# Optimization experiments

Measured on AMD Instinct MI355X. Metric: run time of the kernel, lower is better.

Reference implementation:

```python
import jax, jax.numpy as jnp
import numpy as np

B, L, D, H = 4, 2048, 1024, 16
DH = D // H

def setup_inputs() -> dict:
    key = jax.random.key(0)
    k1, k2, k3 = jax.random.split(key, 3)
    x = jax.random.normal(k1, (B, L, D), dtype=jnp.float32)
    w_qkv = jax.random.normal(k2, (3 * D, D), dtype=jnp.float32) * (1.0 / np.sqrt(D))
    w_proj = jax.random.normal(k3, (D, D), dtype=jnp.float32) * (1.0 / np.sqrt(D))
    return {"x": x, "w_qkv": w_qkv, "w_proj": w_proj}

def reference(x, w_qkv, w_proj):
    b, l, d = x.shape
    scale = 1.0 / np.sqrt(DH)
    qkv = (x @ w_qkv.T).reshape(b, l, 3, H, DH)
    qkv = jnp.transpose(qkv, (2, 0, 3, 1, 4))
    q, k, v = qkv[0], qkv[1], qkv[2]
    scores = jnp.einsum('bhqd,bhkd->bhqk', q, k) * scale
    attn = jax.nn.softmax(scores, axis=-1)
    out = jnp.einsum('bhqk,bhkd->bhqd', attn, v)
    out = jnp.transpose(out, (0, 2, 1, 3)).reshape(b, l, d)
    return out @ w_proj.T
```

## Files before the change

kernel.cpp:

```cpp
#include <hip/hip_runtime.h>
#include <hip/hip_bf16.h>


typedef __bf16  bf16x8  __attribute__((ext_vector_type(8)));
typedef __bf16  bf16x4  __attribute__((ext_vector_type(4)));
typedef float   floatx4 __attribute__((ext_vector_type(4)));

__device__ __forceinline__ void async_ld16(const void* g, void* lds_base_uniform) {
  __builtin_amdgcn_global_load_lds(
      (const __attribute__((address_space(1))) void*)g,
      (__attribute__((address_space(3))) void*)lds_base_uniform,
      16, 0, 0);
}

__device__ __forceinline__ int detect_bf16(const void* p) {
  const unsigned short* u = (const unsigned short*)p;
  int sane = 0;
#pragma unroll 4
  for (int i = 0; i < 64; ++i) {
    unsigned short w = u[2 * i];
    int e = (w >> 7) & 0xFF;
    sane += (w == 0 || (e >= 100 && e <= 150)) ? 1 : 0;
  }
  return sane >= 32;
}

__device__ __forceinline__ bf16x8 ld8_f32cvt(const void* base, size_t elem) {
  const float* p = (const float*)base + elem;
  floatx4 u0 = *(const floatx4*)p;
  floatx4 u1 = *(const floatx4*)(p + 4);
  bf16x8 v;
  v[0] = (__bf16)u0[0]; v[1] = (__bf16)u0[1]; v[2] = (__bf16)u0[2]; v[3] = (__bf16)u0[3];
  v[4] = (__bf16)u1[0]; v[5] = (__bf16)u1[1]; v[6] = (__bf16)u1[2]; v[7] = (__bf16)u1[3];
  return v;
}

template<int CTRL>
__device__ __forceinline__ float dpp_f(float x) {
  return __builtin_bit_cast(float,
      __builtin_amdgcn_update_dpp(0, __builtin_bit_cast(int, x), CTRL, 0xF, 0xF, true));
}
__device__ __forceinline__ float row16_sum(float x) {
  x += dpp_f<0xB1>(x);
  x += dpp_f<0x4E>(x);
  x += dpp_f<0x141>(x);
  x += dpp_f<0x140>(x);
  return x;
}

__launch_bounds__(256)
__global__ void cvt3_kernel(const void* __restrict__ s0, __bf16* __restrict__ d0, int n0,
                            const void* __restrict__ s1, __bf16* __restrict__ d1, int n1,
                            const void* __restrict__ s2, __bf16* __restrict__ d2) {
  int u = blockIdx.x * blockDim.x + threadIdx.x;
  const void* src; __bf16* dst;
  if (u < n0)           { src = s0; dst = d0; }
  else if (u < n0 + n1) { src = s1; dst = d1; u -= n0; }
  else                  { src = s2; dst = d2; u -= n0 + n1; }
  const int is_bf16 = detect_bf16(src);
  const size_t e = (size_t)u * 8;
  if (is_bf16) *(bf16x8*)(dst + e) = *(const bf16x8*)((const __bf16*)src + e);
  else         *(bf16x8*)(dst + e) = ld8_f32cvt(src, e);
}

template<int EPI>
__launch_bounds__(256, 3)
__global__ void gemm_bt_kernel(const __bf16* __restrict__ A,
                               const __bf16* __restrict__ B,
                               const void* __restrict__ oprobe,
                               void* __restrict__ Cout,
                               __bf16* __restrict__ qb,
                               __bf16* __restrict__ kb,
                               __bf16* __restrict__ vtb,
                               int M, int N, int K)
{
  __shared__ __align__(16) __bf16 As[128 * 32];
  __shared__ __align__(16) __bf16 Bs[128 * 32];

  const int flat = blockIdx.x;
  const int m0 = (((flat & 7) << 3) | ((flat >> 3) & 7)) << 7;
  const int n0 = (flat >> 6) << 7;

  const int tid  = threadIdx.x;
  const int wave = tid >> 6;
  const int lane = tid & 63;
  const int quad = lane >> 4;
  const int l16  = lane & 15;
  const int wm   = wave >> 1;
  const int wn   = wave & 1;

  const int r_in   = lane >> 2;
  const int cchunk = lane & 3;

  const __bf16* Ab = A + (size_t)m0 * K;
  const __bf16* Bb = B + (size_t)n0 * K;

  floatx4 acc[4][4];
#pragma unroll
  for (int i = 0; i < 4; ++i)
#pragma unroll
    for (int j = 0; j < 4; ++j)
      acc[i][j] = (floatx4){0.f, 0.f, 0.f, 0.f};

  const int ca0 = wave * 2;
  for (int k0 = 0; k0 < K; k0 += 32) {
#pragma unroll
    for (int i = 0; i < 2; ++i) {
      const int ca  = ca0 + i;
      const int row = ca * 16 + r_in;
      async_ld16(Ab + (size_t)row * K + k0 + cchunk * 8, (char*)As + ca * 1024);
      async_ld16(Bb + (size_t)row * K + k0 + cchunk * 8, (char*)Bs + ca * 1024);
    }
    __syncthreads();

    bf16x8 af[4], bfr[4];
#pragma unroll
    for (int tt = 0; tt < 4; ++tt) {
      af[tt]  = *(const bf16x8*)&As[(wm * 64 + tt * 16 + l16) * 32 + quad * 8];
      bfr[tt] = *(const bf16x8*)&Bs[(wn * 64 + tt * 16 + l16) * 32 + quad * 8];
    }
#pragma unroll
    for (int mt = 0; mt < 4; ++mt)
#pragma unroll
      for (int nt = 0; nt < 4; ++nt)
        acc[mt][nt] = __builtin_amdgcn_mfma_f32_16x16x32_bf16(af[mt], bfr[nt], acc[mt][nt], 0, 0, 0);
    __syncthreads();
  }

  const int out_bf16 = (EPI == 1) ? detect_bf16(oprobe) : 0;

#pragma unroll
  for (int mt = 0; mt < 4; ++mt) {
#pragma unroll
    for (int nt = 0; nt < 4; ++nt) {
      const int n_idx = n0 + wn * 64 + nt * 16 + l16;
      const int mbase = m0 + wm * 64 + mt * 16 + quad * 4;
      if (EPI == 1) {
        if (out_bf16) {
#pragma unroll
          for (int r = 0; r < 4; ++r)
            ((__bf16*)Cout)[(size_t)(mbase + r) * N + n_idx] = (__bf16)acc[mt][nt][r];
        } else {
#pragma unroll
          for (int r = 0; r < 4; ++r)
            ((float*)Cout)[(size_t)(mbase + r) * N + n_idx] = acc[mt][nt][r];
        }
      } else {
        const int sel = n_idx >> 10;
        const int rem = n_idx & 1023;
        const int h   = rem >> 6;
        const int dh  = rem & 63;
        const int b   = mbase >> 11;
        const int l   = mbase & 2047;
        const int bh  = b * 16 + h;
        if (sel == 2) {
          bf16x4 pk;
#pragma unroll
          for (int r = 0; r < 4; ++r) pk[r] = (__bf16)acc[mt][nt][r];
          *(bf16x4*)&vtb[((size_t)bh * 64 + dh) * 2048 + l] = pk;
        } else {
          __bf16* dstb = (sel == 0 ? qb : kb) + ((size_t)bh * 2048 + l) * 64 + dh;
#pragma unroll
          for (int r = 0; r < 4; ++r)
            dstb[(size_t)r * 64] = (__bf16)acc[mt][nt][r];
        }
      }
    }
  }
}

__launch_bounds__(256, 4)
__global__ void attn_kernel(const __bf16* __restrict__ qb,
                            const __bf16* __restrict__ kb,
                            const __bf16* __restrict__ vtb,
                            __bf16* __restrict__ ob )
{
  __shared__ __align__(16) __bf16 S[2][2 * 64 * 72];

  const int tid  = threadIdx.x;
  const int wave = tid >> 6;
  const int lane = tid & 63;
  const int quad = lane >> 4;
  const int l16  = lane & 15;

  const int bh = blockIdx.y;
  const int b  = bh >> 4;
  const int h  = bh & 15;
  const int q0 = blockIdx.x * 128;

  const __bf16* Qp = qb  + (size_t)bh * 2048 * 64;
  const __bf16* Kp = kb  + (size_t)bh * 2048 * 64;
  const __bf16* Vp = vtb + (size_t)bh * 64 * 2048;

  const float C1 = 0.125f * 1.44269504f;
  const float C2 = -8.0f  * 1.44269504f;

  bf16x8 aq[2][2];
#pragma unroll
  for (int rt = 0; rt < 2; ++rt) {
    const __bf16* qrow = Qp + (size_t)(q0 + wave * 32 + rt * 16 + l16) * 64;
    aq[rt][0] = *(const bf16x8*)(qrow + quad * 8);
    aq[rt][1] = *(const bf16x8*)(qrow + 32 + quad * 8);
  }

  bf16x8 onesb;
  {
    const __bf16 ov = (l16 == 0) ? (__bf16)1.0f : (__bf16)0.0f;
#pragma unroll
    for (int i = 0; i < 8; ++i) onesb[i] = ov;
  }

  floatx4 o[2][4], o5[2];
#pragma unroll
  for (int rt = 0; rt < 2; ++rt) {
    o5[rt] = (floatx4){0.f, 0.f, 0.f, 0.f};
#pragma unroll
    for (int dt = 0; dt < 4; ++dt) o[rt][dt] = (floatx4){0.f, 0.f, 0.f, 0.f};
  }

  const int sarr = wave >> 1;
  const int srb  = (wave & 1) * 32;
  const int sr0  = lane >> 3;
  const int scol = (lane & 7) * 8;

  {
    __bf16* dst = &S[0][sarr * (64 * 72)];
    if (sarr == 0) {
#pragma unroll
      for (int i = 0; i < 4; ++i) {
        const int row = srb + sr0 + 8 * i;
        *(bf16x8*)&dst[row * 72 + scol] = *(const bf16x8*)(Kp + (size_t)row * 64 + scol);
      }
    } else {
#pragma unroll
      for (int i = 0; i < 4; ++i) {
        const int row = srb + sr0 + 8 * i;
        *(bf16x8*)&dst[row * 72 + scol] = *(const bf16x8*)(Vp + (size_t)row * 2048 + scol);
      }
    }
  }
  __syncthreads();

  for (int kt = 0; kt < 32; ++kt) {
    const int cur = kt & 1;
    const int nxt = cur ^ 1;
    const int kn  = (((kt + 1) & 31) << 6);

    bf16x8 sreg[4];
    if (sarr == 0) {
#pragma unroll
      for (int i = 0; i < 4; ++i) {
        const int row = srb + sr0 + 8 * i;
        sreg[i] = *(const bf16x8*)(Kp + (size_t)(kn + row) * 64 + scol);
      }
    } else {
#pragma unroll
      for (int i = 0; i < 4; ++i) {
        const int row = srb + sr0 + 8 * i;
        sreg[i] = *(const bf16x8*)(Vp + (size_t)row * 2048 + kn + scol);
      }
    }

    const __bf16* Kc = &S[cur][0];
    const __bf16* Vc = &S[cur][64 * 72];
    __bf16*       Pq = &S[nxt][0] + wave * 2304;

    floatx4 st[2][4];
    __builtin_amdgcn_s_setprio(1);
#pragma unroll
    for (int nt = 0; nt < 4; ++nt) {
      const int krow = nt * 16 + l16;
      bf16x8 ak0 = *(const bf16x8*)&Kc[krow * 72 + quad * 8];
      bf16x8 ak1 = *(const bf16x8*)&Kc[krow * 72 + 32 + quad * 8];
#pragma unroll
      for (int rt = 0; rt < 2; ++rt) {
        floatx4 z = (floatx4){0.f, 0.f, 0.f, 0.f};
        z = __builtin_amdgcn_mfma_f32_16x16x32_bf16(ak0, aq[rt][0], z, 0, 0, 0);
        z = __builtin_amdgcn_mfma_f32_16x16x32_bf16(ak1, aq[rt][1], z, 0, 0, 0);
        st[rt][nt] = z;
      }
    }
    __builtin_amdgcn_s_setprio(0);

#pragma unroll
    for (int rt = 0; rt < 2; ++rt) {
#pragma unroll
      for (int nt = 0; nt < 4; ++nt) {
        bf16x4 pk;
#pragma unroll
        for (int r = 0; r < 4; ++r)
          pk[r] = (__bf16)__builtin_amdgcn_exp2f(fmaf(st[rt][nt][r], C1, C2));
        *(bf16x4*)&Pq[(rt * 16 + l16) * 72 + nt * 16 + quad * 4] = pk;
      }
    }

    __builtin_amdgcn_wave_barrier();

    bf16x8 ap[2][2];
#pragma unroll
    for (int rt = 0; rt < 2; ++rt) {
      ap[rt][0] = *(const bf16x8*)&Pq[(rt * 16 + l16) * 72 + quad * 8];
      ap[rt][1] = *(const bf16x8*)&Pq[(rt * 16 + l16) * 72 + 32 + quad * 8];
    }

    __builtin_amdgcn_s_setprio(1);
#pragma unroll
    for (int dt = 0; dt < 4; ++dt) {
      const int vrow = dt * 16 + l16;
      bf16x8 bv0 = *(const bf16x8*)&Vc[vrow * 72 + quad * 8];
      bf16x8 bv1 = *(const bf16x8*)&Vc[vrow * 72 + 32 + quad * 8];
#pragma unroll
      for (int rt = 0; rt < 2; ++rt) {
        o[rt][dt] = __builtin_amdgcn_mfma_f32_16x16x32_bf16(ap[rt][0], bv0, o[rt][dt], 0, 0, 0);
        o[rt][dt] = __builtin_amdgcn_mfma_f32_16x16x32_bf16(ap[rt][1], bv1, o[rt][dt], 0, 0, 0);
      }
    }
#pragma unroll
    for (int rt = 0; rt < 2; ++rt) {
      o5[rt] = __builtin_amdgcn_mfma_f32_16x16x32_bf16(ap[rt][0], onesb, o5[rt], 0, 0, 0);
      o5[rt] = __builtin_amdgcn_mfma_f32_16x16x32_bf16(ap[rt][1], onesb, o5[rt], 0, 0, 0);
    }
    __builtin_amdgcn_s_setprio(0);

    __builtin_amdgcn_wave_barrier();

    {
      __bf16* dst = &S[nxt][sarr * (64 * 72)];
#pragma unroll
      for (int i = 0; i < 4; ++i) {
        const int row = srb + sr0 + 8 * i;
        *(bf16x8*)&dst[row * 72 + scol] = sreg[i];
      }
    }
    __syncthreads();
  }

#pragma unroll
  for (int rt = 0; rt < 2; ++rt)
#pragma unroll
    for (int r = 0; r < 4; ++r) {
      const float lv  = row16_sum(l16 == 0 ? o5[rt][r] : 0.f);
      const float inv = 1.f / lv;
      const size_t rowbase =
          ((size_t)b * 2048 + q0 + wave * 32 + rt * 16 + quad * 4 + r) * 1024 + h * 64;
#pragma unroll
      for (int dt = 0; dt < 4; ++dt)
        ob[rowbase + dt * 16 + l16] = (__bf16)(o[rt][dt][r] * inv);
    }
}

extern "C" void kernel_launch(void* const* d_in, const int* in_sizes, int n_in,
                              void* d_out, int out_size, void* d_ws, size_t ws_size,
                              hipStream_t stream)
{
  (void)in_sizes; (void)n_in; (void)out_size; (void)ws_size;

  const void* x     = d_in[0];
  const void* wqkv  = d_in[1];
  const void* wproj = d_in[2];

  const size_t NX    = (size_t)8192 * 1024;
  const size_t NWQKV = (size_t)3072 * 1024;
  const size_t NWPRJ = (size_t)1024 * 1024;

  __bf16* qbuf   = (__bf16*)d_ws;
  __bf16* kbuf   = qbuf + NX;
  __bf16* vtbuf  = kbuf + NX;
  __bf16* abuf   = vtbuf + NX;
  __bf16* xb     = abuf + NX;
  __bf16* wqkvb  = xb + NX;
  __bf16* wprojb = wqkvb + NWQKV;

  dim3 blk(256);

  cvt3_kernel<<<dim3((NX + NWQKV + NWPRJ) / 2048), blk, 0, stream>>>(
      x, xb, NX / 8, wqkv, wqkvb, NWQKV / 8, wproj, wprojb);

  gemm_bt_kernel<0><<<dim3(24 * 64), blk, 0, stream>>>(
      xb, wqkvb, nullptr, nullptr, qbuf, kbuf, vtbuf, 8192, 3072, 1024);

  attn_kernel<<<dim3(2048 / 128, 64), blk, 0, stream>>>(qbuf, kbuf, vtbuf, abuf);

  gemm_bt_kernel<1><<<dim3(8 * 64), blk, 0, stream>>>(
      abuf, wprojb, wproj, d_out, nullptr, nullptr, nullptr, 8192, 1024, 1024);
}
```

Measured before the change: 288.1 us.

## Add dedicated 256x256 QKV GEMM kernel with 4-stage async LDS pipeline

```diff
diff --git a/kernel.cpp b/kernel.cpp
--- a/kernel.cpp
+++ b/kernel.cpp
@@ -63,15 +63,115 @@
   else         *(bf16x8*)(dst + e) = ld8_f32cvt(src, e);
 }
 
+__launch_bounds__(512, 2)
+__global__ void gemm_qkv_kernel(const __bf16* __restrict__ A,
+                                const __bf16* __restrict__ B,
+                                __bf16* __restrict__ qb,
+                                __bf16* __restrict__ kb,
+                                __bf16* __restrict__ vtb)
+{
+  __shared__ __align__(16) __bf16 SM[4 * 16384];
+
+  const int flat = blockIdx.x;
+  const int xcd  = flat & 7;
+  const int j    = flat >> 3;
+  const int m0   = ((xcd << 2) | (j & 3)) << 8;
+  const int n0   = (j >> 2) << 8;
+
+  const int tid  = threadIdx.x;
+  const int wave = tid >> 6;
+  const int lane = tid & 63;
+  const int quad = lane >> 4;
+  const int l16  = lane & 15;
+  const int wm   = wave >> 2;
+  const int wn   = wave & 3;
+
+  const int srow = tid >> 2;
+  const int scc  = (((tid & 3) ^ ((tid >> 3) & 3)) << 3);
+
+  auto STAGE = [&](int buf, int k0) {
+    char* base = (char*)SM + buf * 32768;
+#pragma unroll
+    for (int i = 0; i < 2; ++i) {
+      async_ld16(A + (size_t)(m0 + i * 128 + srow) * 1024 + k0 + scc,
+                 base + i * 8192 + wave * 1024);
+      async_ld16(B + (size_t)(n0 + i * 128 + srow) * 1024 + k0 + scc,
+                 base + 16384 + i * 8192 + wave * 1024);
+    }
+  };
+
+  floatx4 acc[8][4];
+#pragma unroll
+  for (int i = 0; i < 8; ++i)
+#pragma unroll
+    for (int n = 0; n < 4; ++n) acc[i][n] = (floatx4){0.f, 0.f, 0.f, 0.f};
+
+  STAGE(0, 0);
+  STAGE(1, 32);
+
+  const int cswz = quad ^ ((l16 >> 1) & 3);
+
+  for (int t = 0; t < 32; ++t) {
+    if (t < 31) asm volatile("s_waitcnt vmcnt(4)" ::: "memory");
+    else        asm volatile("s_waitcnt vmcnt(0)" ::: "memory");
+    __builtin_amdgcn_s_barrier();
+    asm volatile("" ::: "memory");
+
+    if (t + 2 < 32) STAGE((t + 2) & 3, (t + 2) << 5);
+
+    const __bf16* As_ = SM + (t & 3) * 16384;
+    const __bf16* Bs_ = As_ + 8192;
+
+    bf16x8 bfr[4];
+#pragma unroll
+    for (int nf = 0; nf < 4; ++nf)
+      bfr[nf] = *(const bf16x8*)&Bs_[(wn * 64 + nf * 16 + l16) * 32 + cswz * 8];
+
+    __builtin_amdgcn_s_setprio(1);
+#pragma unroll
+    for (int mf = 0; mf < 8; ++mf) {
+      bf16x8 af = *(const bf16x8*)&As_[(wm * 128 + mf * 16 + l16) * 32 + cswz * 8];
+#pragma unroll
+      for (int nf = 0; nf < 4; ++nf)
+        acc[mf][nf] = __builtin_amdgcn_mfma_f32_16x16x32_bf16(af, bfr[nf], acc[mf][nf], 0, 0, 0);
+    }
+    __builtin_amdgcn_s_setprio(0);
+  }
+
+#pragma unroll
+  for (int mf = 0; mf < 8; ++mf) {
+#pragma unroll
+    for (int nf = 0; nf < 4; ++nf) {
+      const int n_idx = n0 + wn * 64 + nf * 16 + l16;
+      const int mbase = m0 + wm * 128 + mf * 16 + quad * 4;
+      const int sel = n_idx >> 10;
+      const int rem = n_idx & 1023;
+      const int h   = rem >> 6;
+      const int dh  = rem & 63;
+      const int b   = mbase >> 11;
+      const int l   = mbase & 2047;
+      const int bh  = b * 16 + h;
+      if (sel == 2) {
+        bf16x4 pk;
+#pragma unroll
+        for (int r = 0; r < 4; ++r) pk[r] = (__bf16)acc[mf][nf][r];
+        *(bf16x4*)&vtb[((size_t)bh * 64 + dh) * 2048 + l] = pk;
+      } else {
+        __bf16* dstb = (sel == 0 ? qb : kb) + ((size_t)bh * 2048 + l) * 64 + dh;
+#pragma unroll
+        for (int r = 0; r < 4; ++r)
+          dstb[(size_t)r * 64] = (__bf16)acc[mf][nf][r];
+      }
+    }
+  }
+}
+
 template<int EPI>
-__launch_bounds__(256, 3)
+__launch_bounds__(256, 2)
 __global__ void gemm_bt_kernel(const __bf16* __restrict__ A,
                                const __bf16* __restrict__ B,
                                const void* __restrict__ oprobe,
                                void* __restrict__ Cout,
-                               __bf16* __restrict__ qb,
-                               __bf16* __restrict__ kb,
-                               __bf16* __restrict__ vtb,
                                int M, int N, int K)
 {
   __shared__ __align__(16) __bf16 As[128 * 32];
@@ -127,7 +227,7 @@
     __syncthreads();
   }
 
-  const int out_bf16 = (EPI == 1) ? detect_bf16(oprobe) : 0;
+  const int out_bf16 = detect_bf16(oprobe);
 
 #pragma unroll
   for (int mt = 0; mt < 4; ++mt) {
@@ -135,35 +235,14 @@
     for (int nt = 0; nt < 4; ++nt) {
       const int n_idx = n0 + wn * 64 + nt * 16 + l16;
       const int mbase = m0 + wm * 64 + mt * 16 + quad * 4;
-      if (EPI == 1) {
-        if (out_bf16) {
-#pragma unroll
-          for (int r = 0; r < 4; ++r)
-            ((__bf16*)Cout)[(size_t)(mbase + r) * N + n_idx] = (__bf16)acc[mt][nt][r];
-        } else {
-#pragma unroll
-          for (int r = 0; r < 4; ++r)
-            ((float*)Cout)[(size_t)(mbase + r) * N + n_idx] = acc[mt][nt][r];
-        }
+      if (out_bf16) {
+#pragma unroll
+        for (int r = 0; r < 4; ++r)
+          ((__bf16*)Cout)[(size_t)(mbase + r) * N + n_idx] = (__bf16)acc[mt][nt][r];
       } else {
-        const int sel = n_idx >> 10;
-        const int rem = n_idx & 1023;
-        const int h   = rem >> 6;
-        const int dh  = rem & 63;
-        const int b   = mbase >> 11;
-        const int l   = mbase & 2047;
-        const int bh  = b * 16 + h;
-        if (sel == 2) {
-          bf16x4 pk;
-#pragma unroll
-          for (int r = 0; r < 4; ++r) pk[r] = (__bf16)acc[mt][nt][r];
-          *(bf16x4*)&vtb[((size_t)bh * 64 + dh) * 2048 + l] = pk;
-        } else {
-          __bf16* dstb = (sel == 0 ? qb : kb) + ((size_t)bh * 2048 + l) * 64 + dh;
-#pragma unroll
-          for (int r = 0; r < 4; ++r)
-            dstb[(size_t)r * 64] = (__bf16)acc[mt][nt][r];
-        }
+#pragma unroll
+        for (int r = 0; r < 4; ++r)
+          ((float*)Cout)[(size_t)(mbase + r) * N + n_idx] = acc[mt][nt][r];
       }
     }
   }
@@ -371,16 +450,14 @@
   __bf16* wqkvb  = xb + NX;
   __bf16* wprojb = wqkvb + NWQKV;
 
-  dim3 blk(256);
-
-  cvt3_kernel<<<dim3((NX + NWQKV + NWPRJ) / 2048), blk, 0, stream>>>(
+  cvt3_kernel<<<dim3((NX + NWQKV + NWPRJ) / 2048), dim3(256), 0, stream>>>(
       x, xb, NX / 8, wqkv, wqkvb, NWQKV / 8, wproj, wprojb);
 
-  gemm_bt_kernel<0><<<dim3(24 * 64), blk, 0, stream>>>(
-      xb, wqkvb, nullptr, nullptr, qbuf, kbuf, vtbuf, 8192, 3072, 1024);
-
-  attn_kernel<<<dim3(2048 / 128, 64), blk, 0, stream>>>(qbuf, kbuf, vtbuf, abuf);
-
-  gemm_bt_kernel<1><<<dim3(8 * 64), blk, 0, stream>>>(
-      abuf, wprojb, wproj, d_out, nullptr, nullptr, nullptr, 8192, 1024, 1024);
-}
+  gemm_qkv_kernel<<<dim3(384), dim3(512), 0, stream>>>(
+      xb, wqkvb, qbuf, kbuf, vtbuf);
+
+  attn_kernel<<<dim3(2048 / 128, 64), dim3(256), 0, stream>>>(qbuf, kbuf, vtbuf, abuf);
+
+  gemm_bt_kernel<1><<<dim3(8 * 64), dim3(256), 0, stream>>>(
+      abuf, wprojb, wproj, d_out, 8192, 1024, 1024);
+}
```

Result: no change. 287.6 us (-0.2%).

## Make GEMMs persistent with 4-buffer async LDS pipeline and swizzled layout

Applied to the files above, without the earlier changes.

```diff
diff --git a/kernel.cpp b/kernel.cpp
--- a/kernel.cpp
+++ b/kernel.cpp
@@ -64,23 +64,19 @@
 }
 
 template<int EPI>
-__launch_bounds__(256, 3)
-__global__ void gemm_bt_kernel(const __bf16* __restrict__ A,
-                               const __bf16* __restrict__ B,
-                               const void* __restrict__ oprobe,
-                               void* __restrict__ Cout,
-                               __bf16* __restrict__ qb,
-                               __bf16* __restrict__ kb,
-                               __bf16* __restrict__ vtb,
-                               int M, int N, int K)
+__launch_bounds__(256, 2)
+__global__ void gemm_ptile_kernel(const __bf16* __restrict__ A,
+                                  const __bf16* __restrict__ B,
+                                  const void* __restrict__ oprobe,
+                                  void* __restrict__ Cout,
+                                  __bf16* __restrict__ qb,
+                                  __bf16* __restrict__ kb,
+                                  __bf16* __restrict__ vtb,
+                                  int ntiles, int N)
 {
-  __shared__ __align__(16) __bf16 As[128 * 32];
-  __shared__ __align__(16) __bf16 Bs[128 * 32];
-
-  const int flat = blockIdx.x;
-  const int m0 = (((flat & 7) << 3) | ((flat >> 3) & 7)) << 7;
-  const int n0 = (flat >> 6) << 7;
-
+  __shared__ __align__(16) __bf16 SM[4 * 8192];
+
+  const int bx   = blockIdx.x;
   const int tid  = threadIdx.x;
   const int wave = tid >> 6;
   const int lane = tid & 63;
@@ -89,80 +85,108 @@
   const int wm   = wave >> 1;
   const int wn   = wave & 1;
 
-  const int r_in   = lane >> 2;
-  const int cchunk = lane & 3;
-
-  const __bf16* Ab = A + (size_t)m0 * K;
-  const __bf16* Bb = B + (size_t)n0 * K;
+  const int tb = ntiles >> 9;
+  const int S  = tb << 5;
+
+  const int srow = tid >> 2;
+  const int scc  = (((tid & 3) ^ ((tid >> 3) & 3)) << 3);
+
+  auto DECODE_M = [&](int t) { return (((t & 7) << 3) | ((t >> 3) & 7)) << 7; };
+  auto DECODE_N = [&](int t) { return (t >> 6) << 7; };
+
+  auto STAGE = [&](int s) {
+    const int t  = bx + ((s >> 5) << 9);
+    const int m0 = DECODE_M(t);
+    const int n0 = DECODE_N(t);
+    const int k0 = (s & 31) << 5;
+    char* base = (char*)SM + (s & 3) * 16384;
+#pragma unroll
+    for (int i = 0; i < 2; ++i) {
+      async_ld16(A + (size_t)(m0 + i * 64 + srow) * 1024 + k0 + scc,
+                 base + i * 4096 + wave * 1024);
+      async_ld16(B + (size_t)(n0 + i * 64 + srow) * 1024 + k0 + scc,
+                 base + 8192 + i * 4096 + wave * 1024);
+    }
+  };
+
+  const int out_bf16 = (EPI == 1) ? detect_bf16(oprobe) : 0;
+  const int cswz = quad ^ ((l16 >> 1) & 3);
 
   floatx4 acc[4][4];
 #pragma unroll
   for (int i = 0; i < 4; ++i)
 #pragma unroll
-    for (int j = 0; j < 4; ++j)
-      acc[i][j] = (floatx4){0.f, 0.f, 0.f, 0.f};
-
-  const int ca0 = wave * 2;
-  for (int k0 = 0; k0 < K; k0 += 32) {
-#pragma unroll
-    for (int i = 0; i < 2; ++i) {
-      const int ca  = ca0 + i;
-      const int row = ca * 16 + r_in;
-      async_ld16(Ab + (size_t)row * K + k0 + cchunk * 8, (char*)As + ca * 1024);
-      async_ld16(Bb + (size_t)row * K + k0 + cchunk * 8, (char*)Bs + ca * 1024);
-    }
-    __syncthreads();
+    for (int j = 0; j < 4; ++j) acc[i][j] = (floatx4){0.f, 0.f, 0.f, 0.f};
+
+  STAGE(0);
+  STAGE(1);
+
+  for (int s = 0; s < S; ++s) {
+    if (s < S - 1) asm volatile("s_waitcnt vmcnt(4)" ::: "memory");
+    else           asm volatile("s_waitcnt vmcnt(0)" ::: "memory");
+    __builtin_amdgcn_s_barrier();
+    asm volatile("" ::: "memory");
+
+    if (s + 2 < S) STAGE(s + 2);
+
+    const __bf16* As_ = SM + (s & 3) * 8192;
+    const __bf16* Bs_ = As_ + 4096;
 
     bf16x8 af[4], bfr[4];
 #pragma unroll
     for (int tt = 0; tt < 4; ++tt) {
-      af[tt]  = *(const bf16x8*)&As[(wm * 64 + tt * 16 + l16) * 32 + quad * 8];
-      bfr[tt] = *(const bf16x8*)&Bs[(wn * 64 + tt * 16 + l16) * 32 + quad * 8];
-    }
+      af[tt]  = *(const bf16x8*)&As_[(wm * 64 + tt * 16 + l16) * 32 + cswz * 8];
+      bfr[tt] = *(const bf16x8*)&Bs_[(wn * 64 + tt * 16 + l16) * 32 + cswz * 8];
+    }
+    __builtin_amdgcn_s_setprio(1);
 #pragma unroll
     for (int mt = 0; mt < 4; ++mt)
 #pragma unroll
       for (int nt = 0; nt < 4; ++nt)
         acc[mt][nt] = __builtin_amdgcn_mfma_f32_16x16x32_bf16(af[mt], bfr[nt], acc[mt][nt], 0, 0, 0);
-    __syncthreads();
-  }
-
-  const int out_bf16 = (EPI == 1) ? detect_bf16(oprobe) : 0;
-
-#pragma unroll
-  for (int mt = 0; mt < 4; ++mt) {
-#pragma unroll
-    for (int nt = 0; nt < 4; ++nt) {
-      const int n_idx = n0 + wn * 64 + nt * 16 + l16;
-      const int mbase = m0 + wm * 64 + mt * 16 + quad * 4;
-      if (EPI == 1) {
-        if (out_bf16) {
-#pragma unroll
-          for (int r = 0; r < 4; ++r)
-            ((__bf16*)Cout)[(size_t)(mbase + r) * N + n_idx] = (__bf16)acc[mt][nt][r];
-        } else {
-#pragma unroll
-          for (int r = 0; r < 4; ++r)
-            ((float*)Cout)[(size_t)(mbase + r) * N + n_idx] = acc[mt][nt][r];
-        }
-      } else {
-        const int sel = n_idx >> 10;
-        const int rem = n_idx & 1023;
-        const int h   = rem >> 6;
-        const int dh  = rem & 63;
-        const int b   = mbase >> 11;
-        const int l   = mbase & 2047;
-        const int bh  = b * 16 + h;
-        if (sel == 2) {
-          bf16x4 pk;
-#pragma unroll
-          for (int r = 0; r < 4; ++r) pk[r] = (__bf16)acc[mt][nt][r];
-          *(bf16x4*)&vtb[((size_t)bh * 64 + dh) * 2048 + l] = pk;
-        } else {
-          __bf16* dstb = (sel == 0 ? qb : kb) + ((size_t)bh * 2048 + l) * 64 + dh;
-#pragma unroll
-          for (int r = 0; r < 4; ++r)
-            dstb[(size_t)r * 64] = (__bf16)acc[mt][nt][r];
+    __builtin_amdgcn_s_setprio(0);
+
+    if ((s & 31) == 31) {
+      const int t  = bx + ((s >> 5) << 9);
+      const int m0 = DECODE_M(t);
+      const int n0 = DECODE_N(t);
+#pragma unroll
+      for (int mt = 0; mt < 4; ++mt) {
+#pragma unroll
+        for (int nt = 0; nt < 4; ++nt) {
+          const int n_idx = n0 + wn * 64 + nt * 16 + l16;
+          const int mbase = m0 + wm * 64 + mt * 16 + quad * 4;
+          if (EPI == 1) {
+            if (out_bf16) {
+#pragma unroll
+              for (int r = 0; r < 4; ++r)
+                ((__bf16*)Cout)[(size_t)(mbase + r) * N + n_idx] = (__bf16)acc[mt][nt][r];
+            } else {
+#pragma unroll
+              for (int r = 0; r < 4; ++r)
+                ((float*)Cout)[(size_t)(mbase + r) * N + n_idx] = acc[mt][nt][r];
+            }
+          } else {
+            const int sel = n_idx >> 10;
+            const int rem = n_idx & 1023;
+            const int h   = rem >> 6;
+            const int dh  = rem & 63;
+            const int b   = mbase >> 11;
+            const int l   = mbase & 2047;
+            const int bh  = b * 16 + h;
+            if (sel == 2) {
+              bf16x4 pk;
+#pragma unroll
+              for (int r = 0; r < 4; ++r) pk[r] = (__bf16)acc[mt][nt][r];
+              *(bf16x4*)&vtb[((size_t)bh * 64 + dh) * 2048 + l] = pk;
+            } else {
+              __bf16* dstb = (sel == 0 ? qb : kb) + ((size_t)bh * 2048 + l) * 64 + dh;
+#pragma unroll
+              for (int r = 0; r < 4; ++r)
+                dstb[(size_t)r * 64] = (__bf16)acc[mt][nt][r];
+            }
+          }
+          acc[mt][nt] = (floatx4){0.f, 0.f, 0.f, 0.f};
         }
       }
     }
@@ -376,11 +400,11 @@
   cvt3_kernel<<<dim3((NX + NWQKV + NWPRJ) / 2048), blk, 0, stream>>>(
       x, xb, NX / 8, wqkv, wqkvb, NWQKV / 8, wproj, wprojb);
 
-  gemm_bt_kernel<0><<<dim3(24 * 64), blk, 0, stream>>>(
-      xb, wqkvb, nullptr, nullptr, qbuf, kbuf, vtbuf, 8192, 3072, 1024);
+  gemm_ptile_kernel<0><<<dim3(512), blk, 0, stream>>>(
+      xb, wqkvb, nullptr, nullptr, qbuf, kbuf, vtbuf, 1536, 3072);
 
   attn_kernel<<<dim3(2048 / 128, 64), blk, 0, stream>>>(qbuf, kbuf, vtbuf, abuf);
 
-  gemm_bt_kernel<1><<<dim3(8 * 64), blk, 0, stream>>>(
-      abuf, wprojb, wproj, d_out, nullptr, nullptr, nullptr, 8192, 1024, 1024);
-}
+  gemm_ptile_kernel<1><<<dim3(512), blk, 0, stream>>>(
+      abuf, wprojb, wproj, d_out, nullptr, nullptr, nullptr, 512, 1024);
+}
```

New measurement: 284.8 us. About the same (-1.1%).
